# Performance work log

Hardware: AMD Instinct MI355X
Metric: run time of the kernel (lower is better)

## Reference

```python
import jax, jax.numpy as jnp
import numpy as np

B, IN_CAPS, IN_DIM = 64, 512, 128
NUM_CAPS, DIM_CAPS, NUM_ROUTING = 32, 32, 3


def squash(x, axis=-1):
    sn = jnp.sum(x * x, axis=axis, keepdims=True)
    return (sn / (1.0 + sn)) * x / (jnp.sqrt(sn) + 1e-8)


def setup_inputs() -> dict:
    key = jax.random.key(0)
    k1, k2, k3 = jax.random.split(key, 3)
    input_tensor = jax.random.normal(k1, (B, IN_CAPS, IN_DIM), dtype=jnp.float32)
    W = 0.001 * jax.random.normal(k2, (NUM_CAPS, IN_DIM, DIM_CAPS), dtype=jnp.float32)
    b0 = jax.random.uniform(k3, (B, NUM_CAPS, IN_CAPS, 1), dtype=jnp.float32)
    return {"input_tensor": input_tensor, "W": W, "b0": b0}


def reference(input_tensor, W, b0):
    # u_hat: (B, num_caps, in_caps, dim_caps)
    u_hat = jnp.einsum('bid,ndc->bnic', input_tensor, W)
    temp_u_hat = jax.lax.stop_gradient(u_hat)
    b = b0
    for _ in range(NUM_ROUTING - 1):
        c = jax.nn.softmax(b, axis=1)            # (B, num_caps, in_caps, 1)
        s = jnp.sum(c * temp_u_hat, axis=2)      # (B, num_caps, dim_caps)
        v = squash(s)
        uv = jnp.einsum('bnic,bnc->bni', temp_u_hat, v)[..., None]
        b = b + uv
    c = jax.nn.softmax(b, axis=1)
    s = jnp.sum(c * u_hat, axis=2)
    return squash(s)                             # (B, num_caps, dim_caps)
```

## Files before the change

kernel.cpp:

```cpp
#include <hip/hip_runtime.h>
#include <math.h>

#define Bsz 64
#define IC  512
#define KD  128
#define NC  32
#define DC  32
#define CHUNK 64
#define NCH   8
#define NBLK  512
#define NTHR  256
#define NTHRB 128

#define CSTR 36
#define BSTR 68
#define WSTR 33

#define CXP_SZ (Bsz * NCH * NC * KD)
#define WV_SZ  (Bsz * NC * KD)

__device__ __forceinline__ int xaddr(int i, int kq) {
    return i * KD + ((((kq) + (i >> 2)) & 31) << 2);
}

__global__ __launch_bounds__(NTHR)
void kACX(const float* __restrict__ bb_in, const float* __restrict__ x_g,
          const float* __restrict__ wv_g, float* __restrict__ bb_out,
          float* __restrict__ cxp, int do_uv, int write_bb)
{
    __shared__ float x_s[CHUNK * KD];
    __shared__ float bb_s[NC * BSTR];
    __shared__ float scr[KD * CSTR];

    const int t = threadIdx.x, blk = blockIdx.x;
    const int b = blk >> 3, ch = blk & 7, i0g = ch * CHUNK;

    for (int rep = 0; rep < 8; ++rep) {
        int v = t + rep * NTHR;
        int i = v >> 5, kq = v & 31;
        *(float4*)(x_s + xaddr(i, kq)) =
            *(const float4*)(x_g + ((size_t)(b * IC + i0g + i)) * KD + (kq << 2));
    }
    for (int rep = 0; rep < 2; ++rep) {
        int v = t + rep * NTHR;
        int n = v >> 4, i4 = v & 15;
        *(float4*)(bb_s + n * BSTR + (i4 << 2)) =
            *(const float4*)(bb_in + ((size_t)(b * NC + n)) * IC + i0g + (i4 << 2));
    }
    if (do_uv) {
        for (int rep = 0; rep < 4; ++rep) {
            const int n = t & 31;
            const int k4 = (t >> 5) + (rep << 3);
            float4 v4 = *(const float4*)(wv_g + ((size_t)(b * NC) + n) * KD + (k4 << 2));
            scr[(k4 * 4 + 0) * CSTR + n] = v4.x;
            scr[(k4 * 4 + 1) * CSTR + n] = v4.y;
            scr[(k4 * 4 + 2) * CSTR + n] = v4.z;
            scr[(k4 * 4 + 3) * CSTR + n] = v4.w;
        }
    }
    __syncthreads();

    if (do_uv) {
        if (t < 128) {
            const int tn = t & 7, ti = t >> 3;
            const int n0 = tn << 2, i0 = ti << 2;
            float4 a0 = {0,0,0,0}, a1 = {0,0,0,0}, a2 = {0,0,0,0}, a3 = {0,0,0,0};
            for (int kq = 0; kq < 32; ++kq) {
                const float4 xr0 = *(const float4*)(x_s + xaddr(i0 + 0, kq));
                const float4 xr1 = *(const float4*)(x_s + xaddr(i0 + 1, kq));
                const float4 xr2 = *(const float4*)(x_s + xaddr(i0 + 2, kq));
                const float4 xr3 = *(const float4*)(x_s + xaddr(i0 + 3, kq));
                const float4 w0 = *(const float4*)(scr + (kq * 4 + 0) * CSTR + n0);
                const float4 w1 = *(const float4*)(scr + (kq * 4 + 1) * CSTR + n0);
                const float4 w2 = *(const float4*)(scr + (kq * 4 + 2) * CSTR + n0);
                const float4 w3 = *(const float4*)(scr + (kq * 4 + 3) * CSTR + n0);
                a0.x += xr0.x*w0.x + xr0.y*w1.x + xr0.z*w2.x + xr0.w*w3.x;
                a0.y += xr0.x*w0.y + xr0.y*w1.y + xr0.z*w2.y + xr0.w*w3.y;
                a0.z += xr0.x*w0.z + xr0.y*w1.z + xr0.z*w2.z + xr0.w*w3.z;
                a0.w += xr0.x*w0.w + xr0.y*w1.w + xr0.z*w2.w + xr0.w*w3.w;
                a1.x += xr1.x*w0.x + xr1.y*w1.x + xr1.z*w2.x + xr1.w*w3.x;
                a1.y += xr1.x*w0.y + xr1.y*w1.y + xr1.z*w2.y + xr1.w*w3.y;
                a1.z += xr1.x*w0.z + xr1.y*w1.z + xr1.z*w2.z + xr1.w*w3.z;
                a1.w += xr1.x*w0.w + xr1.y*w1.w + xr1.z*w2.w + xr1.w*w3.w;
                a2.x += xr2.x*w0.x + xr2.y*w1.x + xr2.z*w2.x + xr2.w*w3.x;
                a2.y += xr2.x*w0.y + xr2.y*w1.y + xr2.z*w2.y + xr2.w*w3.y;
                a2.z += xr2.x*w0.z + xr2.y*w1.z + xr2.z*w2.z + xr2.w*w3.z;
                a2.w += xr2.x*w0.w + xr2.y*w1.w + xr2.z*w2.w + xr2.w*w3.w;
                a3.x += xr3.x*w0.x + xr3.y*w1.x + xr3.z*w2.x + xr3.w*w3.x;
                a3.y += xr3.x*w0.y + xr3.y*w1.y + xr3.z*w2.y + xr3.w*w3.y;
                a3.z += xr3.x*w0.z + xr3.y*w1.z + xr3.z*w2.z + xr3.w*w3.z;
                a3.w += xr3.x*w0.w + xr3.y*w1.w + xr3.z*w2.w + xr3.w*w3.w;
            }
            bb_s[(n0+0)*BSTR + i0+0] += a0.x; bb_s[(n0+1)*BSTR + i0+0] += a0.y;
            bb_s[(n0+2)*BSTR + i0+0] += a0.z; bb_s[(n0+3)*BSTR + i0+0] += a0.w;
            bb_s[(n0+0)*BSTR + i0+1] += a1.x; bb_s[(n0+1)*BSTR + i0+1] += a1.y;
            bb_s[(n0+2)*BSTR + i0+1] += a1.z; bb_s[(n0+3)*BSTR + i0+1] += a1.w;
            bb_s[(n0+0)*BSTR + i0+2] += a2.x; bb_s[(n0+1)*BSTR + i0+2] += a2.y;
            bb_s[(n0+2)*BSTR + i0+2] += a2.z; bb_s[(n0+3)*BSTR + i0+2] += a2.w;
            bb_s[(n0+0)*BSTR + i0+3] += a3.x; bb_s[(n0+1)*BSTR + i0+3] += a3.y;
            bb_s[(n0+2)*BSTR + i0+3] += a3.z; bb_s[(n0+3)*BSTR + i0+3] += a3.w;
        }
        __syncthreads();
        if (write_bb) {
            for (int rep = 0; rep < 2; ++rep) {
                int v = t + rep * NTHR;
                int n = v >> 4, i4 = v & 15;
                *(float4*)(bb_out + ((size_t)(b * NC + n)) * IC + i0g + (i4 << 2)) =
                    *(const float4*)(bb_s + n * BSTR + (i4 << 2));
            }
        }
    }

    if (t < CHUNK) {
        const int ii = t;
        float m = -1e30f;
        #pragma unroll
        for (int n = 0; n < NC; ++n) m = fmaxf(m, bb_s[n * BSTR + ii]);
        float e[NC]; float sum = 0.f;
        #pragma unroll
        for (int n = 0; n < NC; ++n) { float ev = __expf(bb_s[n * BSTR + ii] - m); e[n] = ev; sum += ev; }
        const float inv = 1.f / sum;
        float* crow = scr + ii * CSTR;
        #pragma unroll
        for (int n = 0; n < NC; ++n) crow[n] = e[n] * inv;
    }
    __syncthreads();

    const int tn = t & 7, tk = t >> 3;
    const int n0 = tn << 2;
    float4 acc0 = {0,0,0,0}, acc1 = {0,0,0,0}, acc2 = {0,0,0,0}, acc3 = {0,0,0,0};
    for (int ii = 0; ii < CHUNK; ++ii) {
        const float4 c4 = *(const float4*)(scr + ii * CSTR + n0);
        const float4 x4 = *(const float4*)(x_s + xaddr(ii, tk));
        acc0.x += c4.x*x4.x; acc0.y += c4.x*x4.y; acc0.z += c4.x*x4.z; acc0.w += c4.x*x4.w;
        acc1.x += c4.y*x4.x; acc1.y += c4.y*x4.y; acc1.z += c4.y*x4.z; acc1.w += c4.y*x4.w;
        acc2.x += c4.z*x4.x; acc2.y += c4.z*x4.y; acc2.z += c4.z*x4.z; acc2.w += c4.z*x4.w;
        acc3.x += c4.w*x4.x; acc3.y += c4.w*x4.y; acc3.z += c4.w*x4.z; acc3.w += c4.w*x4.w;
    }
    float* base = cxp + ((size_t)(b * NCH + ch)) * NC * KD + (tk << 2);
    *(float4*)(base + (size_t)(n0 + 0) * KD) = acc0;
    *(float4*)(base + (size_t)(n0 + 1) * KD) = acc1;
    *(float4*)(base + (size_t)(n0 + 2) * KD) = acc2;
    *(float4*)(base + (size_t)(n0 + 3) * KD) = acc3;
}

__global__ __launch_bounds__(NTHRB)
void kB(const float* __restrict__ cxp, const float* __restrict__ W_g,
        float* __restrict__ wv_g, float* __restrict__ out_g, int final_)
{
    __shared__ float w_s[KD * WSTR];
    __shared__ float cxs[4 * KD];
    __shared__ float vs_s[4][DC];

    const int t = threadIdx.x, blk = blockIdx.x;
    const int pb_n = blk & 31, pb_b0 = (blk >> 5) * 4;

    for (int rep = 0; rep < 8; ++rep) {
        int v = t + rep * NTHRB;
        int k = v >> 3, d0 = (v & 7) << 2;
        float4 w4 = *(const float4*)(W_g + (size_t)pb_n * KD * DC + (v << 2));
        float* dst = w_s + k * WSTR + d0;
        dst[0] = w4.x; dst[1] = w4.y; dst[2] = w4.z; dst[3] = w4.w;
    }
    {
        const int bsub = t >> 5, k4 = t & 31;
        float4 s4 = {0,0,0,0};
        const float* p = cxp + (((size_t)(pb_b0 + bsub) * NCH) * NC + pb_n) * KD + (k4 << 2);
        #pragma unroll
        for (int c2 = 0; c2 < NCH; ++c2) {
            float4 v4 = *(const float4*)(p + (size_t)c2 * NC * KD);
            s4.x += v4.x; s4.y += v4.y; s4.z += v4.z; s4.w += v4.w;
        }
        *(float4*)(cxs + bsub * KD + (k4 << 2)) = s4;
    }
    __syncthreads();

    const int bsub = t >> 5, d = t & 31;
    float s = 0.f;
    const float* crow = cxs + bsub * KD;
    for (int k = 0; k < KD; ++k) s += crow[k] * w_s[k * WSTR + d];
    float sn = s * s;
    #pragma unroll
    for (int off = 1; off < 32; off <<= 1) sn += __shfl_xor(sn, off, 64);
    const float vv = s * (sn / ((1.f + sn) * (sqrtf(sn) + 1e-8f)));

    if (final_) {
        out_g[((size_t)(pb_b0 + bsub) * NC + pb_n) * DC + d] = vv;
    } else {
        vs_s[bsub][d] = vv;
        __syncthreads();
        const int k = t;
        float a0 = 0.f, a1 = 0.f, a2 = 0.f, a3 = 0.f;
        #pragma unroll
        for (int dd = 0; dd < DC; ++dd) {
            const float wk = w_s[k * WSTR + dd];
            a0 += wk * vs_s[0][dd];
            a1 += wk * vs_s[1][dd];
            a2 += wk * vs_s[2][dd];
            a3 += wk * vs_s[3][dd];
        }
        size_t base = (((size_t)pb_b0 * NC) + pb_n) * KD + k;
        wv_g[base                      ] = a0;
        wv_g[base + 1 * (size_t)NC * KD] = a1;
        wv_g[base + 2 * (size_t)NC * KD] = a2;
        wv_g[base + 3 * (size_t)NC * KD] = a3;
    }
}

extern "C" void kernel_launch(void* const* d_in, const int* in_sizes, int n_in,
                              void* d_out, int out_size, void* d_ws, size_t ws_size,
                              hipStream_t stream) {
    const float* x  = (const float*)d_in[0];
    const float* W  = (const float*)d_in[1];
    const float* b0 = (const float*)d_in[2];
    float* out = (float*)d_out;

    float* cxp   = (float*)d_ws;
    float* wv    = cxp + CXP_SZ;
    float* bb_ws = wv + WV_SZ;

    kACX<<<NBLK, NTHR, 0, stream>>>(b0, x, nullptr, nullptr, cxp, 0, 0);
    kB  <<<NBLK, NTHRB, 0, stream>>>(cxp, W, wv, out, 0);
    kACX<<<NBLK, NTHR, 0, stream>>>(b0, x, wv, bb_ws, cxp, 1, 1);
    kB  <<<NBLK, NTHRB, 0, stream>>>(cxp, W, wv, out, 0);
    kACX<<<NBLK, NTHR, 0, stream>>>(bb_ws, x, wv, nullptr, cxp, 1, 0);
    kB  <<<NBLK, NTHRB, 0, stream>>>(cxp, W, wv, out, 1);
}
```

Baseline: 127.6 us.

## Fuse routing iterations into one cooperative kernel with per-batch group barriers

Replaces the six alternating kACX/kB launches with a single cooperative kernel. Each block keeps its x chunk and logits in shared memory across all three routing iterations, and the 8 blocks of a batch sync through atomic group barriers in global memory. The squash and W·v projection work is spread across those 8 blocks, so bb no longer has to be written to and reread from global memory. The uv matmul now uses all 256 threads with shared-memory atomics. This removes launch overhead and redundant loads, but adds spin-wait barriers, a memset launch, and the risk of deadlock if the fallback path runs without all blocks co-resident.

```diff
diff --git a/kernel.cpp b/kernel.cpp
--- a/kernel.cpp
+++ b/kernel.cpp
@@ -10,30 +10,44 @@
 #define NCH   8
 #define NBLK  512
 #define NTHR  256
-#define NTHRB 128
+#define GRPBLK 8
 
 #define CSTR 36
 #define BSTR 68
-#define WSTR 33
 
 #define CXP_SZ (Bsz * NCH * NC * KD)
 #define WV_SZ  (Bsz * NC * KD)
+#define NBAR 5
 
 __device__ __forceinline__ int xaddr(int i, int kq) {
     return i * KD + ((((kq) + (i >> 2)) & 31) << 2);
 }
 
-__global__ __launch_bounds__(NTHR)
-void kACX(const float* __restrict__ bb_in, const float* __restrict__ x_g,
-          const float* __restrict__ wv_g, float* __restrict__ bb_out,
-          float* __restrict__ cxp, int do_uv, int write_bb)
+__device__ __forceinline__ void groupbar(unsigned* bar, int idx) {
+    __syncthreads();
+    if (threadIdx.x == 0) {
+        __threadfence();
+        __hip_atomic_fetch_add(&bar[idx], 1u, __ATOMIC_RELEASE, __HIP_MEMORY_SCOPE_AGENT);
+        while (__hip_atomic_load(&bar[idx], __ATOMIC_RELAXED, __HIP_MEMORY_SCOPE_AGENT) < GRPBLK) {
+            __builtin_amdgcn_s_sleep(1);
+        }
+        __threadfence();
+    }
+    __syncthreads();
+}
+
+extern "C" __global__ __launch_bounds__(NTHR, 2)
+void kFused(const float* __restrict__ x_g, const float* __restrict__ W_g,
+            const float* __restrict__ b0_g, float* __restrict__ out_g,
+            float* __restrict__ cxp, float* __restrict__ wv_g,
+            unsigned* __restrict__ bar)
 {
     __shared__ float x_s[CHUNK * KD];
     __shared__ float bb_s[NC * BSTR];
     __shared__ float scr[KD * CSTR];
 
     const int t = threadIdx.x, blk = blockIdx.x;
-    const int b = blk >> 3, ch = blk & 7, i0g = ch * CHUNK;
+    const int b = blk & 63, ch = blk >> 6, i0g = ch * CHUNK;
 
     for (int rep = 0; rep < 8; ++rep) {
         int v = t + rep * NTHR;
@@ -45,165 +59,167 @@
         int v = t + rep * NTHR;
         int n = v >> 4, i4 = v & 15;
         *(float4*)(bb_s + n * BSTR + (i4 << 2)) =
-            *(const float4*)(bb_in + ((size_t)(b * NC + n)) * IC + i0g + (i4 << 2));
-    }
-    if (do_uv) {
-        for (int rep = 0; rep < 4; ++rep) {
-            const int n = t & 31;
-            const int k4 = (t >> 5) + (rep << 3);
-            float4 v4 = *(const float4*)(wv_g + ((size_t)(b * NC) + n) * KD + (k4 << 2));
-            scr[(k4 * 4 + 0) * CSTR + n] = v4.x;
-            scr[(k4 * 4 + 1) * CSTR + n] = v4.y;
-            scr[(k4 * 4 + 2) * CSTR + n] = v4.z;
-            scr[(k4 * 4 + 3) * CSTR + n] = v4.w;
-        }
+            *(const float4*)(b0_g + ((size_t)(b * NC + n)) * IC + i0g + (i4 << 2));
     }
     __syncthreads();
 
-    if (do_uv) {
-        if (t < 128) {
-            const int tn = t & 7, ti = t >> 3;
-            const int n0 = tn << 2, i0 = ti << 2;
-            float4 a0 = {0,0,0,0}, a1 = {0,0,0,0}, a2 = {0,0,0,0}, a3 = {0,0,0,0};
-            for (int kq = 0; kq < 32; ++kq) {
-                const float4 xr0 = *(const float4*)(x_s + xaddr(i0 + 0, kq));
-                const float4 xr1 = *(const float4*)(x_s + xaddr(i0 + 1, kq));
-                const float4 xr2 = *(const float4*)(x_s + xaddr(i0 + 2, kq));
-                const float4 xr3 = *(const float4*)(x_s + xaddr(i0 + 3, kq));
-                const float4 w0 = *(const float4*)(scr + (kq * 4 + 0) * CSTR + n0);
-                const float4 w1 = *(const float4*)(scr + (kq * 4 + 1) * CSTR + n0);
-                const float4 w2 = *(const float4*)(scr + (kq * 4 + 2) * CSTR + n0);
-                const float4 w3 = *(const float4*)(scr + (kq * 4 + 3) * CSTR + n0);
-                a0.x += xr0.x*w0.x + xr0.y*w1.x + xr0.z*w2.x + xr0.w*w3.x;
-                a0.y += xr0.x*w0.y + xr0.y*w1.y + xr0.z*w2.y + xr0.w*w3.y;
-                a0.z += xr0.x*w0.z + xr0.y*w1.z + xr0.z*w2.z + xr0.w*w3.z;
-                a0.w += xr0.x*w0.w + xr0.y*w1.w + xr0.z*w2.w + xr0.w*w3.w;
-                a1.x += xr1.x*w0.x + xr1.y*w1.x + xr1.z*w2.x + xr1.w*w3.x;
-                a1.y += xr1.x*w0.y + xr1.y*w1.y + xr1.z*w2.y + xr1.w*w3.y;
-                a1.z += xr1.x*w0.z + xr1.y*w1.z + xr1.z*w2.z + xr1.w*w3.z;
-                a1.w += xr1.x*w0.w + xr1.y*w1.w + xr1.z*w2.w + xr1.w*w3.w;
-                a2.x += xr2.x*w0.x + xr2.y*w1.x + xr2.z*w2.x + xr2.w*w3.x;
-                a2.y += xr2.x*w0.y + xr2.y*w1.y + xr2.z*w2.y + xr2.w*w3.y;
-                a2.z += xr2.x*w0.z + xr2.y*w1.z + xr2.z*w2.z + xr2.w*w3.z;
-                a2.w += xr2.x*w0.w + xr2.y*w1.w + xr2.z*w2.w + xr2.w*w3.w;
-                a3.x += xr3.x*w0.x + xr3.y*w1.x + xr3.z*w2.x + xr3.w*w3.x;
-                a3.y += xr3.x*w0.y + xr3.y*w1.y + xr3.z*w2.y + xr3.w*w3.y;
-                a3.z += xr3.x*w0.z + xr3.y*w1.z + xr3.z*w2.z + xr3.w*w3.z;
-                a3.w += xr3.x*w0.w + xr3.y*w1.w + xr3.z*w2.w + xr3.w*w3.w;
-            }
-            bb_s[(n0+0)*BSTR + i0+0] += a0.x; bb_s[(n0+1)*BSTR + i0+0] += a0.y;
-            bb_s[(n0+2)*BSTR + i0+0] += a0.z; bb_s[(n0+3)*BSTR + i0+0] += a0.w;
-            bb_s[(n0+0)*BSTR + i0+1] += a1.x; bb_s[(n0+1)*BSTR + i0+1] += a1.y;
-            bb_s[(n0+2)*BSTR + i0+1] += a1.z; bb_s[(n0+3)*BSTR + i0+1] += a1.w;
-            bb_s[(n0+0)*BSTR + i0+2] += a2.x; bb_s[(n0+1)*BSTR + i0+2] += a2.y;
-            bb_s[(n0+2)*BSTR + i0+2] += a2.z; bb_s[(n0+3)*BSTR + i0+2] += a2.w;
-            bb_s[(n0+0)*BSTR + i0+3] += a3.x; bb_s[(n0+1)*BSTR + i0+3] += a3.y;
-            bb_s[(n0+2)*BSTR + i0+3] += a3.z; bb_s[(n0+3)*BSTR + i0+3] += a3.w;
+    int barIdx = 0;
+    for (int it = 0; it < 3; ++it) {
+        if (it > 0) {
+            for (int rep = 0; rep < 4; ++rep) {
+                const int n = t & 31;
+                const int k4 = (t >> 5) + (rep << 3);
+                float4 v4 = *(const float4*)(wv_g + ((size_t)(b * NC) + n) * KD + (k4 << 2));
+                scr[(k4 * 4 + 0) * CSTR + n] = v4.x;
+                scr[(k4 * 4 + 1) * CSTR + n] = v4.y;
+                scr[(k4 * 4 + 2) * CSTR + n] = v4.z;
+                scr[(k4 * 4 + 3) * CSTR + n] = v4.w;
+            }
+            __syncthreads();
+            {
+                const int tt = t & 127;
+                const int tn = tt & 7, ti = tt >> 3;
+                const int n0 = tn << 2, i0 = ti << 2;
+                const int kq0 = (t >> 7) << 4;
+                float4 a0 = {0,0,0,0}, a1 = {0,0,0,0}, a2 = {0,0,0,0}, a3 = {0,0,0,0};
+                for (int kq = kq0; kq < kq0 + 16; ++kq) {
+                    const float4 xr0 = *(const float4*)(x_s + xaddr(i0 + 0, kq));
+                    const float4 xr1 = *(const float4*)(x_s + xaddr(i0 + 1, kq));
+                    const float4 xr2 = *(const float4*)(x_s + xaddr(i0 + 2, kq));
+                    const float4 xr3 = *(const float4*)(x_s + xaddr(i0 + 3, kq));
+                    const float4 w0 = *(const float4*)(scr + (kq * 4 + 0) * CSTR + n0);
+                    const float4 w1 = *(const float4*)(scr + (kq * 4 + 1) * CSTR + n0);
+                    const float4 w2 = *(const float4*)(scr + (kq * 4 + 2) * CSTR + n0);
+                    const float4 w3 = *(const float4*)(scr + (kq * 4 + 3) * CSTR + n0);
+                    a0.x += xr0.x*w0.x + xr0.y*w1.x + xr0.z*w2.x + xr0.w*w3.x;
+                    a0.y += xr0.x*w0.y + xr0.y*w1.y + xr0.z*w2.y + xr0.w*w3.y;
+                    a0.z += xr0.x*w0.z + xr0.y*w1.z + xr0.z*w2.z + xr0.w*w3.z;
+                    a0.w += xr0.x*w0.w + xr0.y*w1.w + xr0.z*w2.w + xr0.w*w3.w;
+                    a1.x += xr1.x*w0.x + xr1.y*w1.x + xr1.z*w2.x + xr1.w*w3.x;
+                    a1.y += xr1.x*w0.y + xr1.y*w1.y + xr1.z*w2.y + xr1.w*w3.y;
+                    a1.z += xr1.x*w0.z + xr1.y*w1.z + xr1.z*w2.z + xr1.w*w3.z;
+                    a1.w += xr1.x*w0.w + xr1.y*w1.w + xr1.z*w2.w + xr1.w*w3.w;
+                    a2.x += xr2.x*w0.x + xr2.y*w1.x + xr2.z*w2.x + xr2.w*w3.x;
+                    a2.y += xr2.x*w0.y + xr2.y*w1.y + xr2.z*w2.y + xr2.w*w3.y;
+                    a2.z += xr2.x*w0.z + xr2.y*w1.z + xr2.z*w2.z + xr2.w*w3.z;
+                    a2.w += xr2.x*w0.w + xr2.y*w1.w + xr2.z*w2.w + xr2.w*w3.w;
+                    a3.x += xr3.x*w0.x + xr3.y*w1.x + xr3.z*w2.x + xr3.w*w3.x;
+                    a3.y += xr3.x*w0.y + xr3.y*w1.y + xr3.z*w2.y + xr3.w*w3.y;
+                    a3.z += xr3.x*w0.z + xr3.y*w1.z + xr3.z*w2.z + xr3.w*w3.z;
+                    a3.w += xr3.x*w0.w + xr3.y*w1.w + xr3.z*w2.w + xr3.w*w3.w;
+                }
+                atomicAdd(&bb_s[(n0+0)*BSTR + i0+0], a0.x);
+                atomicAdd(&bb_s[(n0+1)*BSTR + i0+0], a0.y);
+                atomicAdd(&bb_s[(n0+2)*BSTR + i0+0], a0.z);
+                atomicAdd(&bb_s[(n0+3)*BSTR + i0+0], a0.w);
+                atomicAdd(&bb_s[(n0+0)*BSTR + i0+1], a1.x);
+                atomicAdd(&bb_s[(n0+1)*BSTR + i0+1], a1.y);
+                atomicAdd(&bb_s[(n0+2)*BSTR + i0+1], a1.z);
+                atomicAdd(&bb_s[(n0+3)*BSTR + i0+1], a1.w);
+                atomicAdd(&bb_s[(n0+0)*BSTR + i0+2], a2.x);
+                atomicAdd(&bb_s[(n0+1)*BSTR + i0+2], a2.y);
+                atomicAdd(&bb_s[(n0+2)*BSTR + i0+2], a2.z);
+                atomicAdd(&bb_s[(n0+3)*BSTR + i0+2], a2.w);
+                atomicAdd(&bb_s[(n0+0)*BSTR + i0+3], a3.x);
+                atomicAdd(&bb_s[(n0+1)*BSTR + i0+3], a3.y);
+                atomicAdd(&bb_s[(n0+2)*BSTR + i0+3], a3.z);
+                atomicAdd(&bb_s[(n0+3)*BSTR + i0+3], a3.w);
+            }
+            __syncthreads();
+        }
+
+        if (t < CHUNK) {
+            const int ii = t;
+            float m = -1e30f;
+            #pragma unroll
+            for (int n = 0; n < NC; ++n) m = fmaxf(m, bb_s[n * BSTR + ii]);
+            float e[NC]; float sum = 0.f;
+            #pragma unroll
+            for (int n = 0; n < NC; ++n) { float ev = __expf(bb_s[n * BSTR + ii] - m); e[n] = ev; sum += ev; }
+            const float inv = 1.f / sum;
+            float* crow = scr + ii * CSTR;
+            #pragma unroll
+            for (int n = 0; n < NC; ++n) crow[n] = e[n] * inv;
         }
         __syncthreads();
-        if (write_bb) {
-            for (int rep = 0; rep < 2; ++rep) {
-                int v = t + rep * NTHR;
-                int n = v >> 4, i4 = v & 15;
-                *(float4*)(bb_out + ((size_t)(b * NC + n)) * IC + i0g + (i4 << 2)) =
-                    *(const float4*)(bb_s + n * BSTR + (i4 << 2));
-            }
-        }
-    }
-
-    if (t < CHUNK) {
-        const int ii = t;
-        float m = -1e30f;
-        #pragma unroll
-        for (int n = 0; n < NC; ++n) m = fmaxf(m, bb_s[n * BSTR + ii]);
-        float e[NC]; float sum = 0.f;
-        #pragma unroll
-        for (int n = 0; n < NC; ++n) { float ev = __expf(bb_s[n * BSTR + ii] - m); e[n] = ev; sum += ev; }
-        const float inv = 1.f / sum;
-        float* crow = scr + ii * CSTR;
-        #pragma unroll
-        for (int n = 0; n < NC; ++n) crow[n] = e[n] * inv;
-    }
-    __syncthreads();
-
-    const int tn = t & 7, tk = t >> 3;
-    const int n0 = tn << 2;
-    float4 acc0 = {0,0,0,0}, acc1 = {0,0,0,0}, acc2 = {0,0,0,0}, acc3 = {0,0,0,0};
-    for (int ii = 0; ii < CHUNK; ++ii) {
-        const float4 c4 = *(const float4*)(scr + ii * CSTR + n0);
-        const float4 x4 = *(const float4*)(x_s + xaddr(ii, tk));
-        acc0.x += c4.x*x4.x; acc0.y += c4.x*x4.y; acc0.z += c4.x*x4.z; acc0.w += c4.x*x4.w;
-        acc1.x += c4.y*x4.x; acc1.y += c4.y*x4.y; acc1.z += c4.y*x4.z; acc1.w += c4.y*x4.w;
-        acc2.x += c4.z*x4.x; acc2.y += c4.z*x4.y; acc2.z += c4.z*x4.z; acc2.w += c4.z*x4.w;
-        acc3.x += c4.w*x4.x; acc3.y += c4.w*x4.y; acc3.z += c4.w*x4.z; acc3.w += c4.w*x4.w;
-    }
-    float* base = cxp + ((size_t)(b * NCH + ch)) * NC * KD + (tk << 2);
-    *(float4*)(base + (size_t)(n0 + 0) * KD) = acc0;
-    *(float4*)(base + (size_t)(n0 + 1) * KD) = acc1;
-    *(float4*)(base + (size_t)(n0 + 2) * KD) = acc2;
-    *(float4*)(base + (size_t)(n0 + 3) * KD) = acc3;
-}
-
-__global__ __launch_bounds__(NTHRB)
-void kB(const float* __restrict__ cxp, const float* __restrict__ W_g,
-        float* __restrict__ wv_g, float* __restrict__ out_g, int final_)
-{
-    __shared__ float w_s[KD * WSTR];
-    __shared__ float cxs[4 * KD];
-    __shared__ float vs_s[4][DC];
-
-    const int t = threadIdx.x, blk = blockIdx.x;
-    const int pb_n = blk & 31, pb_b0 = (blk >> 5) * 4;
-
-    for (int rep = 0; rep < 8; ++rep) {
-        int v = t + rep * NTHRB;
-        int k = v >> 3, d0 = (v & 7) << 2;
-        float4 w4 = *(const float4*)(W_g + (size_t)pb_n * KD * DC + (v << 2));
-        float* dst = w_s + k * WSTR + d0;
-        dst[0] = w4.x; dst[1] = w4.y; dst[2] = w4.z; dst[3] = w4.w;
-    }
-    {
-        const int bsub = t >> 5, k4 = t & 31;
-        float4 s4 = {0,0,0,0};
-        const float* p = cxp + (((size_t)(pb_b0 + bsub) * NCH) * NC + pb_n) * KD + (k4 << 2);
-        #pragma unroll
-        for (int c2 = 0; c2 < NCH; ++c2) {
-            float4 v4 = *(const float4*)(p + (size_t)c2 * NC * KD);
-            s4.x += v4.x; s4.y += v4.y; s4.z += v4.z; s4.w += v4.w;
-        }
-        *(float4*)(cxs + bsub * KD + (k4 << 2)) = s4;
-    }
-    __syncthreads();
-
-    const int bsub = t >> 5, d = t & 31;
-    float s = 0.f;
-    const float* crow = cxs + bsub * KD;
-    for (int k = 0; k < KD; ++k) s += crow[k] * w_s[k * WSTR + d];
-    float sn = s * s;
-    #pragma unroll
-    for (int off = 1; off < 32; off <<= 1) sn += __shfl_xor(sn, off, 64);
-    const float vv = s * (sn / ((1.f + sn) * (sqrtf(sn) + 1e-8f)));
-
-    if (final_) {
-        out_g[((size_t)(pb_b0 + bsub) * NC + pb_n) * DC + d] = vv;
-    } else {
-        vs_s[bsub][d] = vv;
-        __syncthreads();
-        const int k = t;
-        float a0 = 0.f, a1 = 0.f, a2 = 0.f, a3 = 0.f;
-        #pragma unroll
-        for (int dd = 0; dd < DC; ++dd) {
-            const float wk = w_s[k * WSTR + dd];
-            a0 += wk * vs_s[0][dd];
-            a1 += wk * vs_s[1][dd];
-            a2 += wk * vs_s[2][dd];
-            a3 += wk * vs_s[3][dd];
-        }
-        size_t base = (((size_t)pb_b0 * NC) + pb_n) * KD + k;
-        wv_g[base                      ] = a0;
-        wv_g[base + 1 * (size_t)NC * KD] = a1;
-        wv_g[base + 2 * (size_t)NC * KD] = a2;
-        wv_g[base + 3 * (size_t)NC * KD] = a3;
+
+        {
+            const int tn = t & 7, tk = t >> 3;
+            const int n0 = tn << 2;
+            float4 acc0 = {0,0,0,0}, acc1 = {0,0,0,0}, acc2 = {0,0,0,0}, acc3 = {0,0,0,0};
+            for (int ii = 0; ii < CHUNK; ++ii) {
+                const float4 c4 = *(const float4*)(scr + ii * CSTR + n0);
+                const float4 x4 = *(const float4*)(x_s + xaddr(ii, tk));
+                acc0.x += c4.x*x4.x; acc0.y += c4.x*x4.y; acc0.z += c4.x*x4.z; acc0.w += c4.x*x4.w;
+                acc1.x += c4.y*x4.x; acc1.y += c4.y*x4.y; acc1.z += c4.y*x4.z; acc1.w += c4.y*x4.w;
+                acc2.x += c4.z*x4.x; acc2.y += c4.z*x4.y; acc2.z += c4.z*x4.z; acc2.w += c4.z*x4.w;
+                acc3.x += c4.w*x4.x; acc3.y += c4.w*x4.y; acc3.z += c4.w*x4.z; acc3.w += c4.w*x4.w;
+            }
+            float* base = cxp + ((size_t)(b * NCH + ch)) * NC * KD + (tk << 2);
+            *(float4*)(base + (size_t)(n0 + 0) * KD) = acc0;
+            *(float4*)(base + (size_t)(n0 + 1) * KD) = acc1;
+            *(float4*)(base + (size_t)(n0 + 2) * KD) = acc2;
+            *(float4*)(base + (size_t)(n0 + 3) * KD) = acc3;
+        }
+
+        groupbar(bar, barIdx * Bsz + b); ++barIdx;
+
+        {
+            const int w = t >> 6, l = t & 63;
+            const int n = (ch << 2) + w;
+            float c0 = 0.f, c1 = 0.f;
+            const float* p = cxp + ((size_t)b * NCH * NC + n) * KD;
+            #pragma unroll
+            for (int c2 = 0; c2 < NCH; ++c2) {
+                c0 += p[(size_t)c2 * NC * KD + l];
+                c1 += p[(size_t)c2 * NC * KD + l + 64];
+            }
+            float* cxs = scr + w * KD;
+            cxs[l] = c0; cxs[l + 64] = c1;
+            __syncthreads();
+            const int dgrp = l & 7, d0 = dgrp << 2, kg = l >> 3;
+            const float* Wn = W_g + (size_t)n * KD * DC;
+            float4 acc = {0,0,0,0};
+            #pragma unroll
+            for (int j = 0; j < 16; ++j) {
+                const int k = (j << 3) + kg;
+                const float4 w4 = *(const float4*)(Wn + (size_t)k * DC + d0);
+                const float cv = cxs[k];
+                acc.x += cv * w4.x; acc.y += cv * w4.y; acc.z += cv * w4.z; acc.w += cv * w4.w;
+            }
+            #pragma unroll
+            for (int off = 8; off < 64; off <<= 1) {
+                acc.x += __shfl_xor(acc.x, off, 64);
+                acc.y += __shfl_xor(acc.y, off, 64);
+                acc.z += __shfl_xor(acc.z, off, 64);
+                acc.w += __shfl_xor(acc.w, off, 64);
+            }
+            float ss = acc.x*acc.x + acc.y*acc.y + acc.z*acc.z + acc.w*acc.w;
+            #pragma unroll
+            for (int off = 1; off < 8; off <<= 1) ss += __shfl_xor(ss, off, 64);
+            const float scale = ss / ((1.f + ss) * (sqrtf(ss) + 1e-8f));
+            float4 v4; v4.x = acc.x*scale; v4.y = acc.y*scale; v4.z = acc.z*scale; v4.w = acc.w*scale;
+
+            if (it == 2) {
+                if (kg == 0) *(float4*)(out_g + ((size_t)(b * NC) + n) * DC + d0) = v4;
+            } else {
+                float* vb = scr + 4 * KD + w * DC;
+                if (kg == 0) *(float4*)(vb + d0) = v4;
+                __threadfence_block();
+                float wv0 = 0.f, wv1 = 0.f;
+                #pragma unroll
+                for (int j = 0; j < 8; ++j) {
+                    const float4 vv = *(const float4*)(vb + (j << 2));
+                    const float4 wa = *(const float4*)(Wn + (size_t)l * DC + (j << 2));
+                    const float4 wb = *(const float4*)(Wn + (size_t)(l + 64) * DC + (j << 2));
+                    wv0 += wa.x*vv.x + wa.y*vv.y + wa.z*vv.z + wa.w*vv.w;
+                    wv1 += wb.x*vv.x + wb.y*vv.y + wb.z*vv.z + wb.w*vv.w;
+                }
+                float* wrow = wv_g + ((size_t)(b * NC) + n) * KD;
+                wrow[l] = wv0; wrow[l + 64] = wv1;
+            }
+        }
+        if (it < 2) { groupbar(bar, barIdx * Bsz + b); ++barIdx; }
     }
 }
 
@@ -215,14 +231,19 @@
     const float* b0 = (const float*)d_in[2];
     float* out = (float*)d_out;
 
-    float* cxp   = (float*)d_ws;
-    float* wv    = cxp + CXP_SZ;
-    float* bb_ws = wv + WV_SZ;
-
-    kACX<<<NBLK, NTHR, 0, stream>>>(b0, x, nullptr, nullptr, cxp, 0, 0);
-    kB  <<<NBLK, NTHRB, 0, stream>>>(cxp, W, wv, out, 0);
-    kACX<<<NBLK, NTHR, 0, stream>>>(b0, x, wv, bb_ws, cxp, 1, 1);
-    kB  <<<NBLK, NTHRB, 0, stream>>>(cxp, W, wv, out, 0);
-    kACX<<<NBLK, NTHR, 0, stream>>>(bb_ws, x, wv, nullptr, cxp, 1, 0);
-    kB  <<<NBLK, NTHRB, 0, stream>>>(cxp, W, wv, out, 1);
-}
+    float* cxp = (float*)d_ws;
+    float* wv  = cxp + CXP_SZ;
+    unsigned* bar = (unsigned*)(wv + WV_SZ);
+
+    hipMemsetAsync(bar, 0, NBAR * Bsz * sizeof(unsigned), stream);
+
+    void* args[] = {(void*)&x, (void*)&W, (void*)&b0, (void*)&out,
+                    (void*)&cxp, (void*)&wv, (void*)&bar};
+    hipError_t err = hipLaunchCooperativeKernel((const void*)kFused, dim3(NBLK), dim3(NTHR),
+                                                args, 0, stream);
+    if (err != hipSuccess) {
+        (void)hipGetLastError();
+        hipLaunchKernelGGL(kFused, dim3(NBLK), dim3(NTHR), 0, stream,
+                           x, W, b0, out, cxp, wv, bar);
+    }
+}
```

New measurement: 323.1 us. 2.53x slower.
